# Optimization experiments

Measured on AMD Instinct MI355X. Metric: run time of the kernel, lower is better.

Reference implementation:

```python
import jax, jax.numpy as jnp
import numpy as np

H, C = 8, 640            # n_heads, sentence_size (per-head out channels)
HC = H * C               # 5120 concatenated head width
NS, NW, NSEC = 8192, 65536, 1024   # sentences, words, sections
EW, ES, ESEC = 131072, 262144, 16384
WORD, SENT, SECT = 300, 640, 512
FFN_HID = 2048


def setup_inputs() -> dict:
    key = jax.random.key(0)
    ks = jax.random.split(key, 32)
    f = lambda k, sh: (jax.random.normal(k, sh, jnp.float32) * 0.02)
    ri = jax.random.randint
    inp = {}
    inp['Hs'] = jax.random.normal(ks[0], (NS, SENT), jnp.float32)
    inp['Hw'] = jax.random.normal(ks[1], (NW, WORD), jnp.float32)
    inp['HS'] = jax.random.normal(ks[2], (NSEC, SECT), jnp.float32)
    # edge_index convention: row 0 = source nodes, row 1 = target (sentence) nodes
    inp['w2s'] = jnp.stack([ri(ks[3], (EW,), 0, NW), ri(ks[4], (EW,), 0, NS)]).astype(jnp.int32)
    inp['s2s'] = jnp.stack([ri(ks[5], (ES,), 0, NS), ri(ks[6], (ES,), 0, NS)]).astype(jnp.int32)
    inp['S2s'] = jnp.stack([ri(ks[7], (ESEC,), 0, NSEC), ri(ks[8], (ESEC,), 0, NS)]).astype(jnp.int32)
    # gat_w: bipartite (word -> sentence)
    inp['Ww_src'] = f(ks[9], (WORD, HC)); inp['Ww_dst'] = f(ks[10], (SENT, HC))
    inp['aw_src'] = f(ks[11], (H, C)); inp['aw_dst'] = f(ks[12], (H, C)); inp['bw'] = f(ks[13], (HC,))
    # gat_s: sentence -> sentence (shared lin for src/dst)
    inp['Ws'] = f(ks[14], (SENT, HC))
    inp['as_src'] = f(ks[15], (H, C)); inp['as_dst'] = f(ks[16], (H, C)); inp['bs'] = f(ks[17], (HC,))
    # gat_S: bipartite (section -> sentence)
    inp['WS_src'] = f(ks[18], (SECT, HC)); inp['WS_dst'] = f(ks[19], (SENT, HC))
    inp['aS_src'] = f(ks[20], (H, C)); inp['aS_dst'] = f(ks[21], (H, C)); inp['bS'] = f(ks[22], (HC,))
    # fusion gates
    inp['F1_w'] = f(ks[23], (2 * HC, HC)); inp['F1_b'] = f(ks[24], (HC,))
    inp['F2_w'] = f(ks[25], (2 * HC, HC)); inp['F2_b'] = f(ks[26], (HC,))
    # FFN
    inp['l1_w'] = f(ks[27], (HC, FFN_HID)); inp['l1_b'] = f(ks[28], (FFN_HID,))
    inp['l2_w'] = f(ks[29], (FFN_HID, SENT)); inp['l2_b'] = f(ks[30], (SENT,))
    return inp


def _gat(xs, xd, Wsrc, Wdst, asrc, adst, b, edge_index):
    """PyG-style GATConv (concat heads), bipartite (xs -> xd)."""
    N = xd.shape[0]
    hs = (xs @ Wsrc).reshape(-1, H, C)          # [Nsrc,H,C]
    hd = (xd @ Wdst).reshape(-1, H, C)          # [Ndst,H,C]
    al_s = jnp.einsum('nhc,hc->nh', hs, asrc)   # [Nsrc,H]
    al_d = jnp.einsum('nhc,hc->nh', hd, adst)   # [Ndst,H]
    src, dst = edge_index[0], edge_index[1]
    e = jax.nn.leaky_relu(al_s[src] + al_d[dst], negative_slope=0.2)  # [E,H]
    m = jax.ops.segment_max(e, dst, num_segments=N)                   # segment-stable softmax
    ex = jnp.exp(e - m[dst])
    den = jax.ops.segment_sum(ex, dst, num_segments=N)
    alpha = ex / (den[dst] + 1e-16)
    out = jax.ops.segment_sum(hs[src] * alpha[:, :, None], dst, num_segments=N)
    return out.reshape(N, HC) + b


def _fusion(X, Y, W, b):
    Z = jax.nn.sigmoid(jnp.concatenate([X, Y], axis=-1) @ W + b)
    return Z * X + (1.0 - Z) * Y


def reference(Hs, Hw, HS, w2s, s2s, S2s,
              Ww_src, Ww_dst, aw_src, aw_dst, bw,
              Ws, as_src, as_dst, bs,
              WS_src, WS_dst, aS_src, aS_dst, bS,
              F1_w, F1_b, F2_w, F2_b,
              l1_w, l1_b, l2_w, l2_b):
    Uw = jax.nn.elu(_gat(Hw, Hs, Ww_src, Ww_dst, aw_src, aw_dst, bw, w2s))
    Us = jax.nn.elu(_gat(Hs, Hs, Ws, Ws, as_src, as_dst, bs, s2s))
    US = jax.nn.elu(_gat(HS, Hs, WS_src, WS_dst, aS_src, aS_dst, bS, S2s))
    U1 = _fusion(Uw, Us, F1_w, F1_b)
    U2 = _fusion(U1, US, F2_w, F2_b)
    return (U2 @ l1_w + l1_b) @ l2_w + l2_b + Hs
```

## Files before the change

### kernel.cpp

```cpp
#include <hip/hip_runtime.h>
#include <cstdint>
#include <cstddef>

typedef __attribute__((ext_vector_type(8))) __bf16 bf16x8;
typedef __attribute__((ext_vector_type(4))) float f32x4;

static constexpr int kNS   = 8192;
static constexpr int kNW   = 65536;
static constexpr int kNSEC = 1024;
static constexpr int kEW   = 131072;
static constexpr int kES   = 262144;
static constexpr int kESEC = 16384;

__device__ __forceinline__ float eluf(float x)  { return x > 0.f ? x : (__expf(x) - 1.f); }
__device__ __forceinline__ float sigmf(float x) { return 1.f / (1.f + __expf(-x)); }

__device__ __forceinline__ void gload16(const __bf16* g, __bf16* l) {
  __builtin_amdgcn_global_load_lds((const __attribute__((address_space(1))) unsigned int*)g,
                                   (__attribute__((address_space(3))) unsigned int*)l,
                                   16, 0, 0);
}

__global__ __launch_bounds__(256) void conv_transpose(const float* __restrict__ W, int K, int N,
                                                      __bf16* __restrict__ Wt, int KP) {
  __shared__ float t[64][33];
  const int nb = blockIdx.x * 32, kb = blockIdx.y * 64;
  const int tx = threadIdx.x & 31, ty = threadIdx.x >> 5;
#pragma unroll
  for (int i = ty; i < 64; i += 8) {
    const int k = kb + i;
    t[i][tx] = (k < K) ? W[(long)k * N + nb + tx] : 0.f;
  }
  __syncthreads();
  union BU { __bf16 b; unsigned short u; };
#pragma unroll
  for (int i = ty; i < 32; i += 8) {
    BU b0, b1;
    b0.b = (__bf16)t[tx * 2][i];
    b1.b = (__bf16)t[tx * 2 + 1][i];
    const unsigned int pk = ((unsigned int)b1.u << 16) | b0.u;
    *(unsigned int*)(Wt + (long)(nb + i) * KP + kb + tx * 2) = pk;
  }
}

__global__ __launch_bounds__(256) void conv_bf4(const float* __restrict__ in, __bf16* __restrict__ outb, long n4) {
  const long i = (long)blockIdx.x * blockDim.x + threadIdx.x;
  if (i >= n4) return;
  const f32x4 v = *(const f32x4*)(in + i * 4);
  union { __bf16 b[4]; uint2 u; } p;
  p.b[0] = (__bf16)v[0]; p.b[1] = (__bf16)v[1];
  p.b[2] = (__bf16)v[2]; p.b[3] = (__bf16)v[3];
  *(uint2*)(outb + i * 4) = p.u;
}

struct HVJ { const float* W; const float* a; float* o; int Kd; int KP; };
struct HVJobs { HVJ j[6]; };

__global__ __launch_bounds__(256) void head_vecs6(HVJobs jb) {
  const HVJ J = jb.j[blockIdx.z];
  const int h = blockIdx.x;
  const int lane = threadIdx.x & 63;
  const int k = blockIdx.y * 4 + (threadIdx.x >> 6);
  if (k >= J.KP) return;
  float s = 0.f;
  if (k < J.Kd) {
    const float* wr = J.W + (long)k * 5120 + h * 640;
    const float* ar = J.a + h * 640;
    for (int c = lane; c < 640; c += 64) s += wr[c] * ar[c];
  }
  for (int o2 = 32; o2; o2 >>= 1) s += __shfl_down(s, o2);
  if (lane == 0) J.o[h * J.KP + k] = (k < J.Kd) ? s : 0.f;
}

__global__ __launch_bounds__(256) void comb_bias(const float* __restrict__ l1_b, const float* __restrict__ l2_w,
                                                 const float* __restrict__ l2_b, float* __restrict__ bc) {
  __shared__ float red[8][32];
  const int no = threadIdx.x & 31;
  const int ko = threadIdx.x >> 5;
  const int n = blockIdx.x * 32 + no;
  float s = 0.f;
  for (int k = ko; k < 2048; k += 8) s += l1_b[k] * l2_w[(long)k * 640 + n];
  red[ko][no] = s;
  __syncthreads();
  if (threadIdx.x < 32) {
    const int nn = blockIdx.x * 32 + threadIdx.x;
    float t = l2_b[nn];
#pragma unroll
    for (int i = 0; i < 8; ++i) t += red[i][threadIdx.x];
    bc[nn] = t;
  }
}

__global__ __launch_bounds__(256) void att_logits(const float* __restrict__ X, int ldx, int Kd,
                                                  const float* __restrict__ vec, int KP,
                                                  float* __restrict__ outl, int N) {
  const int lane = threadIdx.x & 63;
  const int node = blockIdx.x * 4 + (threadIdx.x >> 6);
  if (node >= N) return;
  const float* xr = X + (long)node * ldx;
  float p[8];
#pragma unroll
  for (int h = 0; h < 8; ++h) p[h] = 0.f;
  for (int k = lane; k < Kd; k += 64) {
    const float xv = xr[k];
#pragma unroll
    for (int h = 0; h < 8; ++h) p[h] += xv * vec[h * KP + k];
  }
#pragma unroll
  for (int h = 0; h < 8; ++h) {
    float v = p[h];
    for (int o2 = 32; o2; o2 >>= 1) v += __shfl_down(v, o2);
    if (lane == 0) outl[(long)node * 8 + h] = v;
  }
}

__global__ __launch_bounds__(256) void att_logits4(const float* __restrict__ X,
                                                   const float* __restrict__ v0, const float* __restrict__ v1,
                                                   const float* __restrict__ v2, const float* __restrict__ v3,
                                                   float* __restrict__ o0, float* __restrict__ o1,
                                                   float* __restrict__ o2, float* __restrict__ o3, int N) {
  const int lane = threadIdx.x & 63;
  const int node = blockIdx.x * 4 + (threadIdx.x >> 6);
  if (node >= N) return;
  const float* xr = X + (long)node * 640;
  float p[4][8];
#pragma unroll
  for (int s = 0; s < 4; ++s)
#pragma unroll
    for (int h = 0; h < 8; ++h) p[s][h] = 0.f;
  for (int k = lane; k < 640; k += 64) {
    const float xv = xr[k];
#pragma unroll
    for (int h = 0; h < 8; ++h) {
      p[0][h] += xv * v0[h * 640 + k];
      p[1][h] += xv * v1[h * 640 + k];
      p[2][h] += xv * v2[h * 640 + k];
      p[3][h] += xv * v3[h * 640 + k];
    }
  }
  float* outs[4] = {o0, o1, o2, o3};
#pragma unroll
  for (int s = 0; s < 4; ++s)
#pragma unroll
    for (int h = 0; h < 8; ++h) {
      float v = p[s][h];
      for (int o2v = 32; o2v; o2v >>= 1) v += __shfl_down(v, o2v);
      if (lane == 0) outs[s][(long)node * 8 + h] = v;
    }
}

__global__ __launch_bounds__(256) void edge_count3(const int* __restrict__ d0, int E0, int* __restrict__ c0,
                                                   const int* __restrict__ d1, int E1, int* __restrict__ c1,
                                                   const int* __restrict__ d2, int E2, int* __restrict__ c2) {
  const int gid = blockIdx.x * blockDim.x + threadIdx.x;
  if (gid < E0) atomicAdd(&c0[d0[gid]], 1);
  else if (gid < E0 + E1) atomicAdd(&c1[d1[gid - E0]], 1);
  else if (gid < E0 + E1 + E2) atomicAdd(&c2[d2[gid - E0 - E1]], 1);
}

__global__ __launch_bounds__(1024) void scan_off3(const int* __restrict__ c0, int* __restrict__ o0,
                                                  const int* __restrict__ c1, int* __restrict__ o1,
                                                  const int* __restrict__ c2, int* __restrict__ o2) {
  const int* cnt = blockIdx.x == 0 ? c0 : (blockIdx.x == 1 ? c1 : c2);
  int* offo = blockIdx.x == 0 ? o0 : (blockIdx.x == 1 ? o1 : o2);
  __shared__ int part[1024];
  const int tid = threadIdx.x;
  const int base = tid * 8;
  int loc[8];
  int s = 0;
#pragma unroll
  for (int i = 0; i < 8; ++i) { loc[i] = s; s += cnt[base + i]; }
  part[tid] = s;
  __syncthreads();
  for (int d2 = 1; d2 < 1024; d2 <<= 1) {
    int v = (tid >= d2) ? part[tid - d2] : 0;
    __syncthreads();
    part[tid] += v;
    __syncthreads();
  }
  const int pre = (tid > 0) ? part[tid - 1] : 0;
#pragma unroll
  for (int i = 0; i < 8; ++i) offo[base + i] = pre + loc[i];
  if (tid == 1023) offo[8192] = part[1023];
}

__global__ __launch_bounds__(256) void edge_fill3(
    const int* __restrict__ s0, const int* __restrict__ d0, int E0, const int* __restrict__ of0, int* __restrict__ cu0, int* __restrict__ sr0,
    const int* __restrict__ s1, const int* __restrict__ d1, int E1, const int* __restrict__ of1, int* __restrict__ cu1, int* __restrict__ sr1,
    const int* __restrict__ s2, const int* __restrict__ d2, int E2, const int* __restrict__ of2, int* __restrict__ cu2, int* __restrict__ sr2) {
  const int gid = blockIdx.x * blockDim.x + threadIdx.x;
  if (gid < E0) {
    const int d = d0[gid];
    sr0[of0[d] + atomicAdd(&cu0[d], 1)] = s0[gid];
  } else if (gid < E0 + E1) {
    const int g = gid - E0, d = d1[g];
    sr1[of1[d] + atomicAdd(&cu1[d], 1)] = s1[g];
  } else if (gid < E0 + E1 + E2) {
    const int g = gid - E0 - E1, d = d2[g];
    sr2[of2[d] + atomicAdd(&cu2[d], 1)] = s2[g];
  }
}

template <int FPAD, int F, bool XPH, bool BIASELU>
__global__ __launch_bounds__(256) void gat_agg(const int* __restrict__ seg_off, const int* __restrict__ ssrc,
                                               const float* __restrict__ als, const float* __restrict__ ald,
                                               const float* __restrict__ X, int ldx,
                                               __bf16* __restrict__ outp, int ldo,
                                               const float* __restrict__ bias) {
  constexpr int C4 = F / 4;
  constexpr int ITEMS = 8 * C4;
  constexpr int L = (ITEMS + 255) / 256;
  const int d = blockIdx.x;
  const int tid = threadIdx.x;
  const int o0 = seg_off[d], o1 = seg_off[d + 1];
  const int deg = o1 - o0;
  __shared__ float exl[64][8];
  __shared__ int ssl[64];
  __shared__ float aldd[8];
  __shared__ float den_s[8];
  if (tid < 8) { aldd[tid] = ald[(long)d * 8 + tid]; den_s[tid] = 0.f; }
  f32x4 acc[L];
  int hh[L], xo[L], oo[L];
  bool vld[L];
#pragma unroll
  for (int l = 0; l < L; ++l) {
    const int idx = tid + l * 256;
    vld[l] = (idx < ITEMS);
    const int h = vld[l] ? (idx / C4) : 0;
    const int c = vld[l] ? (idx - h * C4) : 0;
    hh[l] = h;
    xo[l] = (XPH ? h * F : 0) + c * 4;
    oo[l] = h * FPAD + c * 4;
#pragma unroll
    for (int r = 0; r < 4; ++r) acc[l][r] = 0.f;
  }
  __syncthreads();
  for (int base = 0; base < deg; base += 64) {
    const int nc = min(64, deg - base);
    if (tid < nc) ssl[tid] = ssrc[o0 + base + tid];
    __syncthreads();
    for (int t = tid; t < nc * 8; t += 256) {
      const int e = t >> 3, h = t & 7;
      float v = als[(long)ssl[e] * 8 + h] + aldd[h];
      v = v > 0.f ? v : 0.2f * v;
      exl[e][h] = __expf(v);
    }
    __syncthreads();
    if (tid < 8) {
      float s = 0.f;
      for (int e = 0; e < nc; ++e) s += exl[e][tid];
      den_s[tid] += s;
    }
    for (int e = 0; e < nc; ++e) {
      const float* xr = X + (long)ssl[e] * ldx;
      const float* ex8 = exl[e];
#pragma unroll
      for (int l = 0; l < L; ++l)
        if (vld[l]) {
          const f32x4 v = *(const f32x4*)(xr + xo[l]);
          acc[l] += ex8[hh[l]] * v;
        }
    }
    __syncthreads();
  }
#pragma unroll
  for (int l = 0; l < L; ++l) {
    if (!vld[l]) continue;
    const float dinv = 1.f / (den_s[hh[l]] + 1e-16f);
#pragma unroll
    for (int j = 0; j < 4; ++j) {
      float r = acc[l][j] * dinv;
      if constexpr (BIASELU) { r += bias[oo[l] + j]; r = eluf(r); }
      outp[(long)d * ldo + oo[l] + j] = (__bf16)r;
    }
  }
}

template <int FPAD, int F, bool XPH, bool BIASELU>
__global__ __launch_bounds__(256) void gat_agg_bf(const int* __restrict__ seg_off, const int* __restrict__ ssrc,
                                                  const float* __restrict__ als, const float* __restrict__ ald,
                                                  const __bf16* __restrict__ X, int ldx,
                                                  __bf16* __restrict__ outp, int ldo,
                                                  const float* __restrict__ bias) {
  constexpr int C8 = F / 8;
  constexpr int ITEMS = 8 * C8;
  constexpr int L = (ITEMS + 255) / 256;
  const int d = blockIdx.x;
  const int tid = threadIdx.x;
  const int o0 = seg_off[d], o1 = seg_off[d + 1];
  const int deg = o1 - o0;
  __shared__ float exl[64][8];
  __shared__ int ssl[64];
  __shared__ float aldd[8];
  __shared__ float den_s[8];
  if (tid < 8) { aldd[tid] = ald[(long)d * 8 + tid]; den_s[tid] = 0.f; }
  float acc[L][8];
  int hh[L], xo[L], oo[L];
  bool vld[L];
#pragma unroll
  for (int l = 0; l < L; ++l) {
    const int idx = tid + l * 256;
    vld[l] = (idx < ITEMS);
    const int h = vld[l] ? (idx / C8) : 0;
    const int c = vld[l] ? (idx - h * C8) : 0;
    hh[l] = h;
    xo[l] = (XPH ? h * F : 0) + c * 8;
    oo[l] = h * FPAD + c * 8;
#pragma unroll
    for (int r = 0; r < 8; ++r) acc[l][r] = 0.f;
  }
  __syncthreads();
  for (int base = 0; base < deg; base += 64) {
    const int nc = min(64, deg - base);
    if (tid < nc) ssl[tid] = ssrc[o0 + base + tid];
    __syncthreads();
    for (int t = tid; t < nc * 8; t += 256) {
      const int e = t >> 3, h = t & 7;
      float v = als[(long)ssl[e] * 8 + h] + aldd[h];
      v = v > 0.f ? v : 0.2f * v;
      exl[e][h] = __expf(v);
    }
    __syncthreads();
    if (tid < 8) {
      float s = 0.f;
      for (int e = 0; e < nc; ++e) s += exl[e][tid];
      den_s[tid] += s;
    }
    for (int e = 0; e < nc; ++e) {
      const __bf16* xr = X + (long)ssl[e] * ldx;
      const float* ex8 = exl[e];
#pragma unroll
      for (int l = 0; l < L; ++l)
        if (vld[l]) {
          const bf16x8 v = *(const bf16x8*)(xr + xo[l]);
          const float w = ex8[hh[l]];
#pragma unroll
          for (int r = 0; r < 8; ++r) acc[l][r] += w * (float)v[r];
        }
    }
    __syncthreads();
  }
#pragma unroll
  for (int l = 0; l < L; ++l) {
    if (!vld[l]) continue;
    const float dinv = 1.f / (den_s[hh[l]] + 1e-16f);
#pragma unroll
    for (int j = 0; j < 8; ++j) {
      float r = acc[l][j] * dinv;
      if constexpr (BIASELU) { r += bias[oo[l] + j]; r = eluf(r); }
      outp[(long)d * ldo + oo[l] + j] = (__bf16)r;
    }
  }
}

template <int EPI>
__global__ __launch_bounds__(256) void gemm_bt(
    const __bf16* __restrict__ A, int lda, const __bf16* __restrict__ A2, int ksplit,
    const __bf16* __restrict__ Bt, int ldb, int K,
    void* __restrict__ Cout, int ldc,
    const float* __restrict__ bias,
    const __bf16* __restrict__ Xg, const __bf16* __restrict__ Yg, int ldxy,
    const float* __restrict__ Res, int ldres,
    long a_zs, long bt_zs, long c_zs, int b_zs) {
  __shared__ __bf16 sA[2][128 * 32];
  __shared__ __bf16 sB[2][128 * 32];
  const int tid = threadIdx.x;
  const int z = blockIdx.z;
  const int m0 = blockIdx.y * 128, n0 = blockIdx.x * 128;
  const __bf16* Ab = A + (long)z * a_zs;
  const __bf16* A2b = A2 ? A2 + (long)z * a_zs : nullptr;
  const __bf16* Btb = Bt + (long)z * bt_zs;
  const int lane = tid & 63;
  const int wv = tid >> 6, wr = wv >> 1, wc = wv & 1;
  const int fr = lane & 15, fq = lane >> 4;

  const int r0 = tid >> 2, r1 = r0 + 64;
  const int csw = (((tid & 3) ^ ((r0 >> 1) & 3)) * 8);
  const int ldst0 = tid * 8;
  const int ldst1 = 2048 + tid * 8;

  f32x4 acc[4][4];
#pragma unroll
  for (int i = 0; i < 4; ++i)
#pragma unroll
    for (int j = 0; j < 4; ++j)
#pragma unroll
      for (int r = 0; r < 4; ++r) acc[i][j][r] = 0.f;

  const int fsw = (fq ^ ((fr >> 1) & 3)) * 8;
  int aof[4], bof[4];
#pragma unroll
  for (int i = 0; i < 4; ++i) {
    aof[i] = (wr * 64 + i * 16 + fr) * 32 + fsw;
    bof[i] = (wc * 64 + i * 16 + fr) * 32 + fsw;
  }

  const int nkt = K >> 5;
  auto stage = [&](int buf, int kt) {
    const int k0 = kt * 32;
    const __bf16* As = Ab;
    int kr = k0;
    if (A2b && k0 >= ksplit) { As = A2b; kr = k0 - ksplit; }
    gload16(As + (long)(m0 + r0) * lda + kr + csw, &sA[buf][ldst0]);
    gload16(As + (long)(m0 + r1) * lda + kr + csw, &sA[buf][ldst1]);
    gload16(Btb + (long)(n0 + r0) * ldb + k0 + csw, &sB[buf][ldst0]);
    gload16(Btb + (long)(n0 + r1) * ldb + k0 + csw, &sB[buf][ldst1]);
  };

  stage(0, 0);
  for (int kt = 0; kt < nkt; ++kt) {
    const int cur = kt & 1;
    __syncthreads();
    if (kt + 1 < nkt) stage(cur ^ 1, kt + 1);
    bf16x8 af[4], bfv[4];
#pragma unroll
    for (int i = 0; i < 4; ++i) {
      af[i] = *(const bf16x8*)(&sA[cur][aof[i]]);
      bfv[i] = *(const bf16x8*)(&sB[cur][bof[i]]);
    }
#pragma unroll
    for (int i = 0; i < 4; ++i)
#pragma unroll
      for (int j = 0; j < 4; ++j)
        acc[i][j] = __builtin_amdgcn_mfma_f32_16x16x32_bf16(af[i], bfv[j], acc[i][j], 0, 0, 0);
  }

  const float* biasb = bias ? bias + (long)z * b_zs : nullptr;
#pragma unroll
  for (int i = 0; i < 4; ++i) {
#pragma unroll
    for (int j = 0; j < 4; ++j) {
#pragma unroll
      for (int r = 0; r < 4; ++r) {
        const int mm = m0 + wr * 64 + i * 16 + fq * 4 + r;
        const int nn = n0 + wc * 64 + j * 16 + fr;
        const float v = acc[i][j][r];
        const long cidx = (long)mm * ldc + nn + (long)z * c_zs;
        if constexpr (EPI == 0) {
          ((float*)Cout)[cidx] = v;
        } else if constexpr (EPI == 1) {
          ((__bf16*)Cout)[cidx] = (__bf16)eluf(v + biasb[nn]);
        } else if constexpr (EPI == 2) {
          const float zt = sigmf(v + biasb[nn]);
          const float x = (float)Xg[(long)mm * ldxy + nn];
          const float y = (float)Yg[(long)mm * ldxy + nn];
          ((__bf16*)Cout)[cidx] = (__bf16)(zt * x + (1.f - zt) * y);
        } else if constexpr (EPI == 3) {
          ((__bf16*)Cout)[cidx] = (__bf16)(v + biasb[nn]);
        } else if constexpr (EPI == 4) {
          ((float*)Cout)[cidx] = v + biasb[nn] + Res[(long)mm * ldres + nn];
        } else {
          ((__bf16*)Cout)[cidx] = (__bf16)v;
        }
      }
    }
  }
}

template <int EPI>
__global__ __launch_bounds__(512, 2) void gemm256(
    const __bf16* __restrict__ A, int lda, const __bf16* __restrict__ A2, int ksplit,
    const __bf16* __restrict__ Bt, int ldb, int K,
    void* __restrict__ Cout, int ldc,
    const float* __restrict__ bias,
    const __bf16* __restrict__ Xg, const __bf16* __restrict__ Yg, int ldxy,
    int nn_tiles) {
  __shared__ __bf16 sA[2][2][256 * 32];
  __shared__ __bf16 sB[2][2][256 * 32];
  const int tid = threadIdx.x;

  const int nwg = gridDim.x;
  const int lin = blockIdx.x;
  const int qq = nwg >> 3, rr = nwg & 7;
  const int xcd = lin & 7, pos = lin >> 3;
  const int swz = (xcd < rr ? xcd * (qq + 1) : rr * (qq + 1) + (xcd - rr) * qq) + pos;
  const int m0 = (swz / nn_tiles) * 256;
  const int n0 = (swz % nn_tiles) * 256;

  const int lane = tid & 63;
  const int wv = tid >> 6, wm = wv >> 2, wn = wv & 3;
  const int fr = lane & 15, fq = lane >> 4;

  const int srow = tid >> 2;
  const int pslot = tid & 3;

  auto stageA = [&](int bp, int tt, int kk) {
    const int kcol0 = tt * 64 + kk * 32;
    const __bf16* src = A;
    int kc = kcol0;
    if (A2 && kcol0 >= ksplit) { src = A2; kc = kcol0 - ksplit; }
    __bf16* dst = &sA[bp][kk][0];
#pragma unroll
    for (int i = 0; i < 2; ++i) {
      const int r = i * 128 + srow;
      const int l = pslot ^ ((r >> 1) & 3);
      gload16(src + (long)(m0 + r) * lda + kc + l * 8, dst + (i * 512 + tid) * 8);
    }
  };
  auto stageB = [&](int bp, int tt, int kk) {
    const int kcol0 = tt * 64 + kk * 32;
    __bf16* dst = &sB[bp][kk][0];
#pragma unroll
    for (int i = 0; i < 2; ++i) {
      const int r = i * 128 + srow;
      const int l = pslot ^ ((r >> 1) & 3);
      gload16(Bt + (long)(n0 + r) * ldb + kcol0 + l * 8, dst + (i * 512 + tid) * 8);
    }
  };

  int aoff[8], boff[4];
#pragma unroll
  for (int mf = 0; mf < 8; ++mf) {
    const int ra = wm * 128 + mf * 16 + fr;
    aoff[mf] = ra * 32 + ((fq ^ ((ra >> 1) & 3)) * 8);
  }
#pragma unroll
  for (int nf = 0; nf < 4; ++nf) {
    const int rb = wn * 64 + nf * 16 + fr;
    boff[nf] = rb * 32 + ((fq ^ ((rb >> 1) & 3)) * 8);
  }

  f32x4 acc[8][4];
#pragma unroll
  for (int i = 0; i < 8; ++i)
#pragma unroll
    for (int j = 0; j < 4; ++j)
#pragma unroll
      for (int r = 0; r < 4; ++r) acc[i][j][r] = 0.f;

  const int nkt = K >> 6;

  bf16x8 aA[4], aB[4], bA[4], bB[4];

  stageA(0, 0, 0); stageB(0, 0, 0); stageA(0, 0, 1); stageB(0, 0, 1);
  asm volatile("s_waitcnt vmcnt(4)" ::: "memory");
  __builtin_amdgcn_s_barrier();
#pragma unroll
  for (int mf = 0; mf < 4; ++mf) aA[mf] = *(const bf16x8*)(&sA[0][0][aoff[mf]]);
#pragma unroll
  for (int nf = 0; nf < 4; ++nf) bA[nf] = *(const bf16x8*)(&sB[0][0][boff[nf]]);

  for (int t = 0; t < nkt; ++t) {
    const int cb = t & 1, nb = cb ^ 1;
    const bool pf = (t + 1 < nkt);

#pragma unroll
    for (int mf = 0; mf < 4; ++mf) aB[mf] = *(const bf16x8*)(&sA[cb][0][aoff[4 + mf]]);
    if (pf) stageA(nb, t + 1, 0);
    asm volatile("s_waitcnt lgkmcnt(4)" ::: "memory");
    __builtin_amdgcn_sched_barrier(0);
    __builtin_amdgcn_s_setprio(1);
#pragma unroll
    for (int mf = 0; mf < 4; ++mf)
#pragma unroll
      for (int nf = 0; nf < 4; ++nf)
        acc[mf][nf] = __builtin_amdgcn_mfma_f32_16x16x32_bf16(aA[mf], bA[nf], acc[mf][nf], 0, 0, 0);
    __builtin_amdgcn_s_setprio(0);
    __builtin_amdgcn_sched_barrier(0);

    if (pf) stageB(nb, t + 1, 0);
    if (pf) asm volatile("s_waitcnt vmcnt(4)" ::: "memory");
    else    asm volatile("s_waitcnt vmcnt(0)" ::: "memory");
    __builtin_amdgcn_s_barrier();

#pragma unroll
    for (int mf = 0; mf < 4; ++mf) aA[mf] = *(const bf16x8*)(&sA[cb][1][aoff[mf]]);
#pragma unroll
    for (int nf = 0; nf < 4; ++nf) bB[nf] = *(const bf16x8*)(&sB[cb][1][boff[nf]]);
    asm volatile("s_waitcnt lgkmcnt(8)" ::: "memory");
    __builtin_amdgcn_sched_barrier(0);
    __builtin_amdgcn_s_setprio(1);
#pragma unroll
    for (int mf = 0; mf < 4; ++mf)
#pragma unroll
      for (int nf = 0; nf < 4; ++nf)
        acc[4 + mf][nf] = __builtin_amdgcn_mfma_f32_16x16x32_bf16(aB[mf], bA[nf], acc[4 + mf][nf], 0, 0, 0);
    __builtin_amdgcn_s_setprio(0);
    __builtin_amdgcn_sched_barrier(0);

#pragma unroll
    for (int mf = 0; mf < 4; ++mf) aB[mf] = *(const bf16x8*)(&sA[cb][1][aoff[4 + mf]]);
    if (pf) stageA(nb, t + 1, 1);
    asm volatile("s_waitcnt lgkmcnt(4)" ::: "memory");
    __builtin_amdgcn_sched_barrier(0);
    __builtin_amdgcn_s_setprio(1);
#pragma unroll
    for (int mf = 0; mf < 4; ++mf)
#pragma unroll
      for (int nf = 0; nf < 4; ++nf)
        acc[mf][nf] = __builtin_amdgcn_mfma_f32_16x16x32_bf16(aA[mf], bB[nf], acc[mf][nf], 0, 0, 0);
    __builtin_amdgcn_s_setprio(0);
    __builtin_amdgcn_sched_barrier(0);

    if (pf) {
      stageB(nb, t + 1, 1);
      asm volatile("s_waitcnt vmcnt(4)" ::: "memory");
    }
    __builtin_amdgcn_s_barrier();

    if (pf) {
#pragma unroll
      for (int mf = 0; mf < 4; ++mf) aA[mf] = *(const bf16x8*)(&sA[nb][0][aoff[mf]]);
#pragma unroll
      for (int nf = 0; nf < 4; ++nf) bA[nf] = *(const bf16x8*)(&sB[nb][0][boff[nf]]);
      asm volatile("s_waitcnt lgkmcnt(8)" ::: "memory");
    } else {
      asm volatile("s_waitcnt lgkmcnt(0)" ::: "memory");
    }
    __builtin_amdgcn_sched_barrier(0);
    __builtin_amdgcn_s_setprio(1);
#pragma unroll
    for (int mf = 0; mf < 4; ++mf)
#pragma unroll
      for (int nf = 0; nf < 4; ++nf)
        acc[4 + mf][nf] = __builtin_amdgcn_mfma_f32_16x16x32_bf16(aB[mf], bB[nf], acc[4 + mf][nf], 0, 0, 0);
    __builtin_amdgcn_s_setprio(0);
    __builtin_amdgcn_sched_barrier(0);
  }

#pragma unroll
  for (int mf = 0; mf < 8; ++mf) {
#pragma unroll
    for (int nf = 0; nf < 4; ++nf) {
#pragma unroll
      for (int r = 0; r < 4; ++r) {
        const int mm = m0 + wm * 128 + mf * 16 + fq * 4 + r;
        const int nn = n0 + wn * 64 + nf * 16 + fr;
        const float v = acc[mf][nf][r];
        const long cidx = (long)mm * ldc + nn;
        if constexpr (EPI == 2) {
          const float zt = sigmf(v + bias[nn]);
          const float x = (float)Xg[(long)mm * ldxy + nn];
          const float y = (float)Yg[(long)mm * ldxy + nn];
          ((__bf16*)Cout)[cidx] = (__bf16)(zt * x + (1.f - zt) * y);
        } else {
          ((__bf16*)Cout)[cidx] = (__bf16)(v + bias[nn]);
        }
      }
    }
  }
}

extern "C" void kernel_launch(void* const* d_in, const int* in_sizes, int n_in,
                              void* d_out, int out_size, void* d_ws, size_t ws_size,
                              hipStream_t stream) {
  (void)in_sizes; (void)n_in; (void)out_size;
  const float* Hs    = (const float*)d_in[0];
  const float* Hw    = (const float*)d_in[1];
  const float* HSec  = (const float*)d_in[2];
  const int* w2s     = (const int*)d_in[3];
  const int* s2s     = (const int*)d_in[4];
  const int* S2s     = (const int*)d_in[5];
  const float* Ww_src = (const float*)d_in[6];
  const float* Ww_dst = (const float*)d_in[7];
  const float* aw_src = (const float*)d_in[8];
  const float* aw_dst = (const float*)d_in[9];
  const float* bw     = (const float*)d_in[10];
  const float* Wss    = (const float*)d_in[11];
  const float* as_src = (const float*)d_in[12];
  const float* as_dst = (const float*)d_in[13];
  const float* bs     = (const float*)d_in[14];
  const float* WS_src = (const float*)d_in[15];
  const float* WS_dst = (const float*)d_in[16];
  const float* aS_src = (const float*)d_in[17];
  const float* aS_dst = (const float*)d_in[18];
  const float* bS     = (const float*)d_in[19];
  const float* F1_w   = (const float*)d_in[20];
  const float* F1_b   = (const float*)d_in[21];
  const float* F2_w   = (const float*)d_in[22];
  const float* F2_b   = (const float*)d_in[23];
  const float* l1_w   = (const float*)d_in[24];
  const float* l1_b   = (const float*)d_in[25];
  const float* l2_w   = (const float*)d_in[26];
  const float* l2_b   = (const float*)d_in[27];
  float* outp = (float*)d_out;

  char* ws = (char*)d_ws;
  size_t cur_off = 0;
  auto alloc = [&](size_t bytes) -> char* {
    char* p = ws + cur_off;
    cur_off = (cur_off + bytes + 255) & ~(size_t)255;
    return p;
  };

  __bf16* Wt_w  = (__bf16*)alloc((size_t)5120 * 320 * 2);
  __bf16* Wt_s  = (__bf16*)alloc((size_t)5120 * 640 * 2);
  __bf16* Wt_S  = (__bf16*)alloc((size_t)5120 * 512 * 2);
  __bf16* WtF   = (__bf16*)alloc((size_t)5120 * 10240 * 2);
  __bf16* Wt_l2 = (__bf16*)alloc((size_t)640 * 2048 * 2);
  __bf16* l1_bf = (__bf16*)alloc((size_t)5120 * 2048 * 2);
  __bf16* WcT   = (__bf16*)alloc((size_t)640 * 5120 * 2);
  float*  bc    = (float*)alloc(640 * 4);
  __bf16* HS_bf = (__bf16*)alloc((size_t)1024 * 512 * 2);
  __bf16* Hs_bf = (__bf16*)alloc((size_t)kNS * 640 * 2);
  float* v_w = (float*)alloc(8 * 320 * 4);
  float* u_w = (float*)alloc(8 * 640 * 4);
  float* v_s = (float*)alloc(8 * 640 * 4);
  float* u_s = (float*)alloc(8 * 640 * 4);
  float* v_S = (float*)alloc(8 * 512 * 4);
  float* u_S = (float*)alloc(8 * 640 * 4);
  float* alw_s = (float*)alloc((size_t)kNW * 8 * 4);
  float* alw_d = (float*)alloc((size_t)kNS * 8 * 4);
  float* als_s = (float*)alloc((size_t)kNS * 8 * 4);
  float* als_d = (float*)alloc((size_t)kNS * 8 * 4);
  float* alS_s = (float*)alloc((size_t)kNSEC * 8 * 4);
  float* alS_d = (float*)alloc((size_t)kNS * 8 * 4);
  int* csr_i  = (int*)alloc((size_t)6 * kNS * 4);
  int* cnt_w = csr_i, *cnt_s = csr_i + kNS, *cnt_S = csr_i + 2 * kNS;
  int* cur_w = csr_i + 3 * kNS, *cur_s = csr_i + 4 * kNS, *cur_S = csr_i + 5 * kNS;
  int* off_w = (int*)alloc((size_t)(kNS + 1) * 4);
  int* off_s = (int*)alloc((size_t)(kNS + 1) * 4);
  int* off_S = (int*)alloc((size_t)(kNS + 1) * 4);
  int* ssrc_w = (int*)alloc((size_t)kEW * 4);
  int* ssrc_s = (int*)alloc((size_t)kES * 4);
  int* ssrc_S = (int*)alloc((size_t)kESEC * 4);
  __bf16* hs_Sb = (__bf16*)alloc((size_t)1024 * 5120 * 2);
  char* aggreg = alloc((size_t)kNS * 2560 * 2 + (size_t)kNS * 5120 * 2);
  __bf16* agg_w = (__bf16*)aggreg;
  __bf16* agg_s = (__bf16*)(aggreg + (size_t)kNS * 2560 * 2);
  __bf16* U1 = (__bf16*)aggreg;
  __bf16* Uw = (__bf16*)alloc((size_t)kNS * 5120 * 2);
  __bf16* Us = (__bf16*)alloc((size_t)kNS * 5120 * 2);
  __bf16* US = (__bf16*)alloc((size_t)kNS * 5120 * 2);
  __bf16* U2 = Uw;

  __bf16* WtF2 = nullptr;
  {
    const size_t f2b = (size_t)5120 * 10240 * 2;
    if (cur_off + f2b + 256 <= ws_size) WtF2 = (__bf16*)alloc(f2b);
  }

  const dim3 b256(256);

  conv_transpose<<<dim3(160, 5), b256, 0, stream>>>(Ww_src, 300, 5120, Wt_w, 320);
  conv_transpose<<<dim3(160, 10), b256, 0, stream>>>(Wss, 640, 5120, Wt_s, 640);
  conv_transpose<<<dim3(160, 8), b256, 0, stream>>>(WS_src, 512, 5120, Wt_S, 512);
  conv_transpose<<<dim3(160, 160), b256, 0, stream>>>(F1_w, 10240, 5120, WtF, 10240);
  if (WtF2) conv_transpose<<<dim3(160, 160), b256, 0, stream>>>(F2_w, 10240, 5120, WtF2, 10240);
  conv_transpose<<<dim3(20, 32), b256, 0, stream>>>(l2_w, 2048, 640, Wt_l2, 2048);
  conv_bf4<<<(1024 * 512 / 4 + 255) / 256, b256, 0, stream>>>(HSec, HS_bf, (long)1024 * 512 / 4);
  conv_bf4<<<((long)kNS * 640 / 4 + 255) / 256, b256, 0, stream>>>(Hs, Hs_bf, (long)kNS * 640 / 4);
  conv_bf4<<<((long)5120 * 2048 / 4 + 255) / 256, b256, 0, stream>>>(l1_w, l1_bf, (long)5120 * 2048 / 4);

  gemm_bt<5><<<dim3(40, 5, 1), b256, 0, stream>>>(
      Wt_l2, 2048, nullptr, 1 << 30, l1_bf, 2048, 2048,
      WcT, 5120, nullptr, nullptr, nullptr, 0, nullptr, 0, 0, 0, 0, 0);
  comb_bias<<<20, b256, 0, stream>>>(l1_b, l2_w, l2_b, bc);

  {
    HVJobs jb;
    jb.j[0] = {Ww_src, aw_src, v_w, 300, 320};
    jb.j[1] = {Ww_dst, aw_dst, u_w, 640, 640};
    jb.j[2] = {Wss,    as_src, v_s, 640, 640};
    jb.j[3] = {Wss,    as_dst, u_s, 640, 640};
    jb.j[4] = {WS_src, aS_src, v_S, 512, 512};
    jb.j[5] = {WS_dst, aS_dst, u_S, 640, 640};
    head_vecs6<<<dim3(8, 160, 6), b256, 0, stream>>>(jb);
  }

  att_logits<<<(kNW + 3) / 4, b256, 0, stream>>>(Hw, 300, 300, v_w, 320, alw_s, kNW);
  att_logits<<<(kNSEC + 3) / 4, b256, 0, stream>>>(HSec, 512, 512, v_S, 512, alS_s, kNSEC);
  att_logits4<<<(kNS + 3) / 4, b256, 0, stream>>>(Hs, u_w, v_s, u_s, u_S,
                                                  alw_d, als_s, als_d, alS_d, kNS);

  hipMemsetAsync(csr_i, 0, (size_t)6 * kNS * 4, stream);
  edge_count3<<<(kEW + kES + kESEC + 255) / 256, b256, 0, stream>>>(
      w2s + kEW, kEW, cnt_w, s2s + kES, kES, cnt_s, S2s + kESEC, kESEC, cnt_S);
  scan_off3<<<3, 1024, 0, stream>>>(cnt_w, off_w, cnt_s, off_s, cnt_S, off_S);
  edge_fill3<<<(kEW + kES + kESEC + 255) / 256, b256, 0, stream>>>(
      w2s, w2s + kEW, kEW, off_w, cur_w, ssrc_w,
      s2s, s2s + kES, kES, off_s, cur_s, ssrc_s,
      S2s, S2s + kESEC, kESEC, off_S, cur_S, ssrc_S);

  gemm_bt<5><<<dim3(40, 8, 1), b256, 0, stream>>>(
      HS_bf, 512, nullptr, 1 << 30, Wt_S, 512, 512,
      hs_Sb, 5120, nullptr, nullptr, nullptr, 0, nullptr, 0, 0, 0, 0, 0);

  gat_agg<320, 300, false, false><<<kNS, b256, 0, stream>>>(off_w, ssrc_w, alw_s, alw_d, Hw, 300, agg_w, 2560, nullptr);
  gat_agg_bf<640, 640, false, false><<<kNS, b256, 0, stream>>>(off_s, ssrc_s, als_s, als_d, Hs_bf, 640, agg_s, 5120, nullptr);
  gat_agg_bf<640, 640, true, true><<<kNS, b256, 0, stream>>>(off_S, ssrc_S, alS_s, alS_d, hs_Sb, 5120, US, 5120, bS);

  gemm_bt<1><<<dim3(5, 64, 8), b256, 0, stream>>>(
      agg_w, 2560, nullptr, 1 << 30, Wt_w, 320, 320,
      Uw, 5120, bw, nullptr, nullptr, 0, nullptr, 0, 320, (long)640 * 320, 640, 640);
  gemm_bt<1><<<dim3(5, 64, 8), b256, 0, stream>>>(
      agg_s, 5120, nullptr, 1 << 30, Wt_s, 640, 640,
      Us, 5120, bs, nullptr, nullptr, 0, nullptr, 0, 640, (long)640 * 640, 640, 640);

  gemm256<2><<<dim3(640), dim3(512), 0, stream>>>(
      Uw, 5120, Us, 5120, WtF, 10240, 10240,
      U1, 5120, F1_b, Uw, Us, 5120, 20);

  if (!WtF2) conv_transpose<<<dim3(160, 160), b256, 0, stream>>>(F2_w, 10240, 5120, WtF, 10240);
  gemm256<2><<<dim3(640), dim3(512), 0, stream>>>(
      U1, 5120, US, 5120, WtF2 ? WtF2 : WtF, 10240, 10240,
      U2, 5120, F2_b, U1, US, 5120, 20);

  gemm_bt<4><<<dim3(5, 64, 1), b256, 0, stream>>>(
      U2, 5120, nullptr, 1 << 30, WcT, 5120, 5120,
      outp, 640, bc, nullptr, nullptr, 0, Hs, 640, 0, 0, 0, 0);
}
```

Measured before the change: 2.875 ms.

## Split-K the tail wave of fusion GEMMs to balance CU occupancy

```diff
diff --git a/kernel.cpp b/kernel.cpp
--- a/kernel.cpp
+++ b/kernel.cpp
@@ -464,18 +464,29 @@
     void* __restrict__ Cout, int ldc,
     const float* __restrict__ bias,
     const __bf16* __restrict__ Xg, const __bf16* __restrict__ Yg, int ldxy,
-    int nn_tiles) {
+    int nn_tiles, int nfull, float* __restrict__ part, int* __restrict__ cnt) {
   __shared__ __bf16 sA[2][2][256 * 32];
   __shared__ __bf16 sB[2][2][256 * 32];
   const int tid = threadIdx.x;
-
-  const int nwg = gridDim.x;
   const int lin = blockIdx.x;
-  const int qq = nwg >> 3, rr = nwg & 7;
-  const int xcd = lin & 7, pos = lin >> 3;
-  const int swz = (xcd < rr ? xcd * (qq + 1) : rr * (qq + 1) + (xcd - rr) * qq) + pos;
-  const int m0 = (swz / nn_tiles) * 256;
-  const int n0 = (swz % nn_tiles) * 256;
+
+  int tile, tbase, nkt, khalf = 0;
+  bool isfull;
+  if (lin < nfull) {
+    const int qq = nfull >> 3, rr = nfull & 7;
+    const int xcd = lin & 7, pos = lin >> 3;
+    tile = (xcd < rr ? xcd * (qq + 1) : rr * (qq + 1) + (xcd - rr) * qq) + pos;
+    tbase = 0; nkt = K >> 6; isfull = true;
+  } else {
+    const int h = lin - nfull;
+    tile = nfull + (h >> 1);
+    khalf = h & 1;
+    nkt = (K >> 6) >> 1;
+    tbase = khalf * nkt;
+    isfull = false;
+  }
+  const int m0 = (tile / nn_tiles) * 256;
+  const int n0 = (tile % nn_tiles) * 256;
 
   const int lane = tid & 63;
   const int wv = tid >> 6, wm = wv >> 2, wn = wv & 3;
@@ -484,8 +495,8 @@
   const int srow = tid >> 2;
   const int pslot = tid & 3;
 
-  auto stageA = [&](int bp, int tt, int kk) {
-    const int kcol0 = tt * 64 + kk * 32;
+  auto stageA = [&](int bp, int kt_abs, int kk) {
+    const int kcol0 = kt_abs * 64 + kk * 32;
     const __bf16* src = A;
     int kc = kcol0;
     if (A2 && kcol0 >= ksplit) { src = A2; kc = kcol0 - ksplit; }
@@ -497,8 +508,8 @@
       gload16(src + (long)(m0 + r) * lda + kc + l * 8, dst + (i * 512 + tid) * 8);
     }
   };
-  auto stageB = [&](int bp, int tt, int kk) {
-    const int kcol0 = tt * 64 + kk * 32;
+  auto stageB = [&](int bp, int kt_abs, int kk) {
+    const int kcol0 = kt_abs * 64 + kk * 32;
     __bf16* dst = &sB[bp][kk][0];
 #pragma unroll
     for (int i = 0; i < 2; ++i) {
@@ -528,11 +539,9 @@
 #pragma unroll
       for (int r = 0; r < 4; ++r) acc[i][j][r] = 0.f;
 
-  const int nkt = K >> 6;
-
   bf16x8 aA[4], aB[4], bA[4], bB[4];
 
-  stageA(0, 0, 0); stageB(0, 0, 0); stageA(0, 0, 1); stageB(0, 0, 1);
+  stageA(0, tbase, 0); stageB(0, tbase, 0); stageA(0, tbase, 1); stageB(0, tbase, 1);
   asm volatile("s_waitcnt vmcnt(4)" ::: "memory");
   __builtin_amdgcn_s_barrier();
 #pragma unroll
@@ -543,10 +552,11 @@
   for (int t = 0; t < nkt; ++t) {
     const int cb = t & 1, nb = cb ^ 1;
     const bool pf = (t + 1 < nkt);
+    const int nxt = tbase + t + 1;
 
 #pragma unroll
     for (int mf = 0; mf < 4; ++mf) aB[mf] = *(const bf16x8*)(&sA[cb][0][aoff[4 + mf]]);
-    if (pf) stageA(nb, t + 1, 0);
+    if (pf) stageA(nb, nxt, 0);
     asm volatile("s_waitcnt lgkmcnt(4)" ::: "memory");
     __builtin_amdgcn_sched_barrier(0);
     __builtin_amdgcn_s_setprio(1);
@@ -558,7 +568,7 @@
     __builtin_amdgcn_s_setprio(0);
     __builtin_amdgcn_sched_barrier(0);
 
-    if (pf) stageB(nb, t + 1, 0);
+    if (pf) stageB(nb, nxt, 0);
     if (pf) asm volatile("s_waitcnt vmcnt(4)" ::: "memory");
     else    asm volatile("s_waitcnt vmcnt(0)" ::: "memory");
     __builtin_amdgcn_s_barrier();
@@ -580,7 +590,7 @@
 
 #pragma unroll
     for (int mf = 0; mf < 4; ++mf) aB[mf] = *(const bf16x8*)(&sA[cb][1][aoff[4 + mf]]);
-    if (pf) stageA(nb, t + 1, 1);
+    if (pf) stageA(nb, nxt, 1);
     asm volatile("s_waitcnt lgkmcnt(4)" ::: "memory");
     __builtin_amdgcn_sched_barrier(0);
     __builtin_amdgcn_s_setprio(1);
@@ -593,7 +603,7 @@
     __builtin_amdgcn_sched_barrier(0);
 
     if (pf) {
-      stageB(nb, t + 1, 1);
+      stageB(nb, nxt, 1);
       asm volatile("s_waitcnt vmcnt(4)" ::: "memory");
     }
     __builtin_amdgcn_s_barrier();
@@ -616,6 +626,28 @@
         acc[4 + mf][nf] = __builtin_amdgcn_mfma_f32_16x16x32_bf16(aB[mf], bB[nf], acc[4 + mf][nf], 0, 0, 0);
     __builtin_amdgcn_s_setprio(0);
     __builtin_amdgcn_sched_barrier(0);
+  }
+
+  if (!isfull) {
+    float* slot = part + ((long)(tile - nfull) * 2 + khalf) * 65536;
+#pragma unroll
+    for (int mf = 0; mf < 8; ++mf)
+#pragma unroll
+      for (int nf = 0; nf < 4; ++nf)
+        *(f32x4*)(slot + ((long)(mf * 4 + nf) * 512 + tid) * 4) = acc[mf][nf];
+    __threadfence();
+    __shared__ int oldv;
+    __syncthreads();
+    if (tid == 0) oldv = atomicAdd(&cnt[tile - nfull], 1);
+    __syncthreads();
+    if (oldv == 0) return;
+    __threadfence();
+    const float* pslot = part + ((long)(tile - nfull) * 2 + (khalf ^ 1)) * 65536;
+#pragma unroll
+    for (int mf = 0; mf < 8; ++mf)
+#pragma unroll
+      for (int nf = 0; nf < 4; ++nf)
+        acc[mf][nf] += *(const f32x4*)(pslot + ((long)(mf * 4 + nf) * 512 + tid) * 4);
   }
 
 #pragma unroll
@@ -724,6 +756,14 @@
   __bf16* US = (__bf16*)alloc((size_t)kNS * 5120 * 2);
   __bf16* U2 = Uw;
 
+  float* skp = nullptr; int* skc = nullptr;
+  {
+    const size_t skp_b = (size_t)128 * 2 * 65536 * 4;
+    if (cur_off + skp_b + 1024 + 512 <= ws_size) {
+      skp = (float*)alloc(skp_b);
+      skc = (int*)alloc(1024);
+    }
+  }
   __bf16* WtF2 = nullptr;
   {
     const size_t f2b = (size_t)5120 * 10240 * 2;
@@ -731,6 +771,8 @@
   }
 
   const dim3 b256(256);
+
+  if (skc) hipMemsetAsync(skc, 0, 1024, stream);
 
   conv_transpose<<<dim3(160, 5), b256, 0, stream>>>(Ww_src, 300, 5120, Wt_w, 320);
   conv_transpose<<<dim3(160, 10), b256, 0, stream>>>(Wss, 640, 5120, Wt_s, 640);
@@ -787,14 +829,26 @@
       agg_s, 5120, nullptr, 1 << 30, Wt_s, 640, 640,
       Us, 5120, bs, nullptr, nullptr, 0, nullptr, 0, 640, (long)640 * 640, 640, 640);
 
-  gemm256<2><<<dim3(640), dim3(512), 0, stream>>>(
-      Uw, 5120, Us, 5120, WtF, 10240, 10240,
-      U1, 5120, F1_b, Uw, Us, 5120, 20);
+  if (skp) {
+    gemm256<2><<<dim3(768), dim3(512), 0, stream>>>(
+        Uw, 5120, Us, 5120, WtF, 10240, 10240,
+        U1, 5120, F1_b, Uw, Us, 5120, 20, 512, skp, skc);
+  } else {
+    gemm256<2><<<dim3(640), dim3(512), 0, stream>>>(
+        Uw, 5120, Us, 5120, WtF, 10240, 10240,
+        U1, 5120, F1_b, Uw, Us, 5120, 20, 640, nullptr, nullptr);
+  }
 
   if (!WtF2) conv_transpose<<<dim3(160, 160), b256, 0, stream>>>(F2_w, 10240, 5120, WtF, 10240);
-  gemm256<2><<<dim3(640), dim3(512), 0, stream>>>(
-      U1, 5120, US, 5120, WtF2 ? WtF2 : WtF, 10240, 10240,
-      U2, 5120, F2_b, U1, US, 5120, 20);
+  if (skp) {
+    gemm256<2><<<dim3(768), dim3(512), 0, stream>>>(
+        U1, 5120, US, 5120, WtF2 ? WtF2 : WtF, 10240, 10240,
+        U2, 5120, F2_b, U1, US, 5120, 20, 512, skp, skc + 128);
+  } else {
+    gemm256<2><<<dim3(640), dim3(512), 0, stream>>>(
+        U1, 5120, US, 5120, WtF2 ? WtF2 : WtF, 10240, 10240,
+        U2, 5120, F2_b, U1, US, 5120, 20, 640, nullptr, nullptr);
+  }
 
   gemm_bt<4><<<dim3(5, 64, 1), b256, 0, stream>>>(
       U2, 5120, nullptr, 1 << 30, WcT, 5120, 5120,
```

Measured after the change: 2.896 ms. No clear change (+0.7%).

## Shrink fusion GEMM tile to 128x256 and restructure the k-loop pipeline

Applied to the files above, without the earlier changes.

```diff
diff --git a/kernel.cpp b/kernel.cpp
--- a/kernel.cpp
+++ b/kernel.cpp
@@ -458,14 +458,14 @@
 }
 
 template <int EPI>
-__global__ __launch_bounds__(512, 2) void gemm256(
+__global__ __launch_bounds__(512, 2) void gemm128(
     const __bf16* __restrict__ A, int lda, const __bf16* __restrict__ A2, int ksplit,
     const __bf16* __restrict__ Bt, int ldb, int K,
     void* __restrict__ Cout, int ldc,
     const float* __restrict__ bias,
     const __bf16* __restrict__ Xg, const __bf16* __restrict__ Yg, int ldxy,
     int nn_tiles) {
-  __shared__ __bf16 sA[2][2][256 * 32];
+  __shared__ __bf16 sA[2][2][128 * 32];
   __shared__ __bf16 sB[2][2][256 * 32];
   const int tid = threadIdx.x;
 
@@ -474,7 +474,7 @@
   const int qq = nwg >> 3, rr = nwg & 7;
   const int xcd = lin & 7, pos = lin >> 3;
   const int swz = (xcd < rr ? xcd * (qq + 1) : rr * (qq + 1) + (xcd - rr) * qq) + pos;
-  const int m0 = (swz / nn_tiles) * 256;
+  const int m0 = (swz / nn_tiles) * 128;
   const int n0 = (swz % nn_tiles) * 256;
 
   const int lane = tid & 63;
@@ -484,21 +484,16 @@
   const int srow = tid >> 2;
   const int pslot = tid & 3;
 
-  auto stageA = [&](int bp, int tt, int kk) {
-    const int kcol0 = tt * 64 + kk * 32;
+  auto stageA = [&](int bp, int kt, int kk) {
+    const int kcol0 = kt * 64 + kk * 32;
     const __bf16* src = A;
     int kc = kcol0;
     if (A2 && kcol0 >= ksplit) { src = A2; kc = kcol0 - ksplit; }
-    __bf16* dst = &sA[bp][kk][0];
-#pragma unroll
-    for (int i = 0; i < 2; ++i) {
-      const int r = i * 128 + srow;
-      const int l = pslot ^ ((r >> 1) & 3);
-      gload16(src + (long)(m0 + r) * lda + kc + l * 8, dst + (i * 512 + tid) * 8);
-    }
+    const int l = pslot ^ ((srow >> 1) & 3);
+    gload16(src + (long)(m0 + srow) * lda + kc + l * 8, &sA[bp][kk][tid * 8]);
   };
-  auto stageB = [&](int bp, int tt, int kk) {
-    const int kcol0 = tt * 64 + kk * 32;
+  auto stageB = [&](int bp, int kt, int kk) {
+    const int kcol0 = kt * 64 + kk * 32;
     __bf16* dst = &sB[bp][kk][0];
 #pragma unroll
     for (int i = 0; i < 2; ++i) {
@@ -508,10 +503,10 @@
     }
   };
 
-  int aoff[8], boff[4];
-#pragma unroll
-  for (int mf = 0; mf < 8; ++mf) {
-    const int ra = wm * 128 + mf * 16 + fr;
+  int aoff[4], boff[4];
+#pragma unroll
+  for (int mf = 0; mf < 4; ++mf) {
+    const int ra = wm * 64 + mf * 16 + fr;
     aoff[mf] = ra * 32 + ((fq ^ ((ra >> 1) & 3)) * 8);
   }
 #pragma unroll
@@ -520,9 +515,9 @@
     boff[nf] = rb * 32 + ((fq ^ ((rb >> 1) & 3)) * 8);
   }
 
-  f32x4 acc[8][4];
-#pragma unroll
-  for (int i = 0; i < 8; ++i)
+  f32x4 acc[4][4];
+#pragma unroll
+  for (int i = 0; i < 4; ++i)
 #pragma unroll
     for (int j = 0; j < 4; ++j)
 #pragma unroll
@@ -533,7 +528,7 @@
   bf16x8 aA[4], aB[4], bA[4], bB[4];
 
   stageA(0, 0, 0); stageB(0, 0, 0); stageA(0, 0, 1); stageB(0, 0, 1);
-  asm volatile("s_waitcnt vmcnt(4)" ::: "memory");
+  asm volatile("s_waitcnt vmcnt(3)" ::: "memory");
   __builtin_amdgcn_s_barrier();
 #pragma unroll
   for (int mf = 0; mf < 4; ++mf) aA[mf] = *(const bf16x8*)(&sA[0][0][aoff[mf]]);
@@ -544,10 +539,16 @@
     const int cb = t & 1, nb = cb ^ 1;
     const bool pf = (t + 1 < nkt);
 
-#pragma unroll
-    for (int mf = 0; mf < 4; ++mf) aB[mf] = *(const bf16x8*)(&sA[cb][0][aoff[4 + mf]]);
-    if (pf) stageA(nb, t + 1, 0);
-    asm volatile("s_waitcnt lgkmcnt(4)" ::: "memory");
+    if (pf) { stageA(nb, t + 1, 0); stageB(nb, t + 1, 0); }
+    if (pf) asm volatile("s_waitcnt vmcnt(3)" ::: "memory");
+    else    asm volatile("s_waitcnt vmcnt(0)" ::: "memory");
+    __builtin_amdgcn_s_barrier();
+
+#pragma unroll
+    for (int mf = 0; mf < 4; ++mf) aB[mf] = *(const bf16x8*)(&sA[cb][1][aoff[mf]]);
+#pragma unroll
+    for (int nf = 0; nf < 4; ++nf) bB[nf] = *(const bf16x8*)(&sB[cb][1][boff[nf]]);
+    asm volatile("s_waitcnt lgkmcnt(8)" ::: "memory");
     __builtin_amdgcn_sched_barrier(0);
     __builtin_amdgcn_s_setprio(1);
 #pragma unroll
@@ -558,43 +559,9 @@
     __builtin_amdgcn_s_setprio(0);
     __builtin_amdgcn_sched_barrier(0);
 
-    if (pf) stageB(nb, t + 1, 0);
-    if (pf) asm volatile("s_waitcnt vmcnt(4)" ::: "memory");
-    else    asm volatile("s_waitcnt vmcnt(0)" ::: "memory");
-    __builtin_amdgcn_s_barrier();
-
-#pragma unroll
-    for (int mf = 0; mf < 4; ++mf) aA[mf] = *(const bf16x8*)(&sA[cb][1][aoff[mf]]);
-#pragma unroll
-    for (int nf = 0; nf < 4; ++nf) bB[nf] = *(const bf16x8*)(&sB[cb][1][boff[nf]]);
-    asm volatile("s_waitcnt lgkmcnt(8)" ::: "memory");
-    __builtin_amdgcn_sched_barrier(0);
-    __builtin_amdgcn_s_setprio(1);
-#pragma unroll
-    for (int mf = 0; mf < 4; ++mf)
-#pragma unroll
-      for (int nf = 0; nf < 4; ++nf)
-        acc[4 + mf][nf] = __builtin_amdgcn_mfma_f32_16x16x32_bf16(aB[mf], bA[nf], acc[4 + mf][nf], 0, 0, 0);
-    __builtin_amdgcn_s_setprio(0);
-    __builtin_amdgcn_sched_barrier(0);
-
-#pragma unroll
-    for (int mf = 0; mf < 4; ++mf) aB[mf] = *(const bf16x8*)(&sA[cb][1][aoff[4 + mf]]);
-    if (pf) stageA(nb, t + 1, 1);
-    asm volatile("s_waitcnt lgkmcnt(4)" ::: "memory");
-    __builtin_amdgcn_sched_barrier(0);
-    __builtin_amdgcn_s_setprio(1);
-#pragma unroll
-    for (int mf = 0; mf < 4; ++mf)
-#pragma unroll
-      for (int nf = 0; nf < 4; ++nf)
-        acc[mf][nf] = __builtin_amdgcn_mfma_f32_16x16x32_bf16(aA[mf], bB[nf], acc[mf][nf], 0, 0, 0);
-    __builtin_amdgcn_s_setprio(0);
-    __builtin_amdgcn_sched_barrier(0);
-
     if (pf) {
-      stageB(nb, t + 1, 1);
-      asm volatile("s_waitcnt vmcnt(4)" ::: "memory");
+      stageA(nb, t + 1, 1); stageB(nb, t + 1, 1);
+      asm volatile("s_waitcnt vmcnt(3)" ::: "memory");
     }
     __builtin_amdgcn_s_barrier();
 
@@ -613,18 +580,18 @@
     for (int mf = 0; mf < 4; ++mf)
 #pragma unroll
       for (int nf = 0; nf < 4; ++nf)
-        acc[4 + mf][nf] = __builtin_amdgcn_mfma_f32_16x16x32_bf16(aB[mf], bB[nf], acc[4 + mf][nf], 0, 0, 0);
+        acc[mf][nf] = __builtin_amdgcn_mfma_f32_16x16x32_bf16(aB[mf], bB[nf], acc[mf][nf], 0, 0, 0);
     __builtin_amdgcn_s_setprio(0);
     __builtin_amdgcn_sched_barrier(0);
   }
 
 #pragma unroll
-  for (int mf = 0; mf < 8; ++mf) {
+  for (int mf = 0; mf < 4; ++mf) {
 #pragma unroll
     for (int nf = 0; nf < 4; ++nf) {
 #pragma unroll
       for (int r = 0; r < 4; ++r) {
-        const int mm = m0 + wm * 128 + mf * 16 + fq * 4 + r;
+        const int mm = m0 + wm * 64 + mf * 16 + fq * 4 + r;
         const int nn = n0 + wn * 64 + nf * 16 + fr;
         const float v = acc[mf][nf][r];
         const long cidx = (long)mm * ldc + nn;
@@ -787,12 +754,12 @@
       agg_s, 5120, nullptr, 1 << 30, Wt_s, 640, 640,
       Us, 5120, bs, nullptr, nullptr, 0, nullptr, 0, 640, (long)640 * 640, 640, 640);
 
-  gemm256<2><<<dim3(640), dim3(512), 0, stream>>>(
+  gemm128<2><<<dim3(1280), dim3(512), 0, stream>>>(
       Uw, 5120, Us, 5120, WtF, 10240, 10240,
       U1, 5120, F1_b, Uw, Us, 5120, 20);
 
   if (!WtF2) conv_transpose<<<dim3(160, 160), b256, 0, stream>>>(F2_w, 10240, 5120, WtF, 10240);
-  gemm256<2><<<dim3(640), dim3(512), 0, stream>>>(
+  gemm128<2><<<dim3(1280), dim3(512), 0, stream>>>(
       U1, 5120, US, 5120, WtF2 ? WtF2 : WtF, 10240, 10240,
       U2, 5120, F2_b, U1, US, 5120, 20);
 
```

Result: slower. 3.709 ms (+29.0%).
